# Optimization experiments

Measured on AMD Instinct MI355X. Metric: run time of the kernel, lower is better.

Reference implementation:

```python
import jax, jax.numpy as jnp
import numpy as np

NUM_HEADS = 16
EMB_SIZE = 1024
HEAD_SIZE = 64


def setup_inputs() -> dict:
    key = jax.random.key(0)
    ks = jax.random.split(key, 9)
    H, E, D = NUM_HEADS, EMB_SIZE, HEAD_SIZE
    s = 1.0 / np.sqrt(E)
    X = jax.random.normal(ks[0], (4, 2048, E), dtype=jnp.float32)
    Wq = jax.random.uniform(ks[1], (H, E, D), jnp.float32, -s, s)
    Wk = jax.random.uniform(ks[2], (H, E, D), jnp.float32, -s, s)
    Wv = jax.random.uniform(ks[3], (H, E, D), jnp.float32, -s, s)
    bq = jax.random.uniform(ks[4], (H, D), jnp.float32, -s, s)
    bk = jax.random.uniform(ks[5], (H, D), jnp.float32, -s, s)
    bv = jax.random.uniform(ks[6], (H, D), jnp.float32, -s, s)
    so = 1.0 / np.sqrt(H * D)
    Wo = jax.random.uniform(ks[7], (H * D, E), jnp.float32, -so, so)
    bo = jax.random.uniform(ks[8], (E,), jnp.float32, -so, so)
    return {"X": X, "Wq": Wq, "Wk": Wk, "Wv": Wv, "bq": bq, "bk": bk, "bv": bv, "Wo": Wo, "bo": bo}


def reference(X, Wq, Wk, Wv, bq, bk, bv, Wo, bo):
    B, S, E = X.shape
    H, _, D = Wq.shape
    # per-head projections (batched over heads)
    q = jnp.einsum('bse,hed->bhsd', X, Wq) + bq[None, :, None, :]
    k = jnp.einsum('bse,hed->bhsd', X, Wk) + bk[None, :, None, :]
    v = jnp.einsum('bse,hed->bhsd', X, Wv) + bv[None, :, None, :]
    # causal scaled-dot-product attention
    scores = jnp.einsum('bhsd,bhtd->bhst', q, k) / jnp.sqrt(jnp.float32(D))
    causal = jnp.tril(jnp.ones((S, S), dtype=bool))
    scores = jnp.where(causal[None, None], scores, jnp.float32(-jnp.inf))
    probs = jax.nn.softmax(scores, axis=-1)
    out = jnp.einsum('bhst,bhtd->bhsd', probs, v)
    # concat heads (head h occupies slots [h*D:(h+1)*D]) then output proj
    concat = out.transpose(0, 2, 1, 3).reshape(B, S, H * D)
    # dropout is identity in eval mode
    return concat @ Wo + bo
```

## Files before the change

kernel.cpp:

```cpp
#include <hip/hip_runtime.h>
#include <stdint.h>


typedef float   f32x4  __attribute__((ext_vector_type(4)));
typedef __bf16  bf16x8 __attribute__((ext_vector_type(8)));
typedef short   short8 __attribute__((ext_vector_type(8)));
typedef unsigned short ushort4v __attribute__((ext_vector_type(4)));

typedef __attribute__((address_space(1))) void GV;
typedef __attribute__((address_space(3))) void LV;

#define DEVI static __device__ __forceinline__

DEVI unsigned short f2bf(float f){
  unsigned u = __float_as_uint(f);
  unsigned r = u + 0x7fffu + ((u>>16)&1u);
  return (unsigned short)(r>>16);
}

DEVI unsigned cvt_pk_bf16(float lo, float hi){
  unsigned r;
  asm("v_cvt_pk_bf16_f32 %0, %1, %2" : "=v"(r) : "v"(lo), "v"(hi));
  return r;
}

DEVI void permlane32_swap(unsigned &a, unsigned &b){
  asm volatile("v_permlane32_swap_b32 %0, %1" : "+v"(a), "+v"(b));
}
DEVI void permlane16_swap(unsigned &a, unsigned &b){
  asm volatile("v_permlane16_swap_b32 %0, %1" : "+v"(a), "+v"(b));
}

DEVI void gl_lds16(const void* g, void* l){
  __builtin_amdgcn_global_load_lds((GV*)g, (LV*)l, 16, 0, 0);
}

#define BAR() asm volatile("s_barrier" ::: "memory")

__global__ __launch_bounds__(256) void pack_x(const float* __restrict__ X,
                                              short* __restrict__ Xb){
  int i = blockIdx.x*256 + threadIdx.x;
  const float4* p = (const float4*)(X + (size_t)i*8);
  float4 a = p[0], b = p[1];
  short8 o;
  o[0]=(short)f2bf(a.x); o[1]=(short)f2bf(a.y); o[2]=(short)f2bf(a.z); o[3]=(short)f2bf(a.w);
  o[4]=(short)f2bf(b.x); o[5]=(short)f2bf(b.y); o[6]=(short)f2bf(b.z); o[7]=(short)f2bf(b.w);
  *(short8*)(Xb + (size_t)i*8) = o;
}

__global__ __launch_bounds__(256) void pack_wqkv(const float* __restrict__ Wq,
                                                 const float* __restrict__ Wk,
                                                 const float* __restrict__ Wv,
                                                 short* __restrict__ Wp){
  int t = blockIdx.x*256 + threadIdx.x;
  int n = t >> 7, kc = t & 127;
  int which = n >> 10, hd = n & 1023, h = hd >> 6, d = hd & 63;
  const float* W = which==0 ? Wq : (which==1 ? Wk : Wv);
  const float* src = W + ((size_t)h*1024 + kc*8)*64 + d;
  short8 o;
  #pragma unroll
  for (int j=0;j<8;++j) o[j] = (short)f2bf(src[(size_t)j*64]);
  *(short8*)(Wp + (size_t)n*1024 + kc*8) = o;
}

__global__ __launch_bounds__(256) void pack_wo(const float* __restrict__ Wo,
                                               short* __restrict__ WoT){
  int t = blockIdx.x*256 + threadIdx.x;
  int n = t >> 7, kc = t & 127;
  const float* src = Wo + (size_t)(kc*8)*1024 + n;
  short8 o;
  #pragma unroll
  for (int j=0;j<8;++j) o[j] = (short)f2bf(src[(size_t)j*1024]);
  *(short8*)(WoT + (size_t)n*1024 + kc*8) = o;
}

__global__ __launch_bounds__(512)
void gemm_qkv(const short* __restrict__ A, const short* __restrict__ Bt,
              const float* __restrict__ b0, const float* __restrict__ b1,
              const float* __restrict__ b2,
              short* __restrict__ Qb, short* __restrict__ Kb, short* __restrict__ Vtb)
{
  __shared__ __align__(16) char sm[4][32768];
  const int K2 = 2048;
  int t = threadIdx.x, lane = t & 63, wid = t >> 6;
  int wr = wid >> 2, wc = wid & 3;
  int l15 = lane & 15, l4 = lane >> 4;
  int swz = (blockIdx.x & 7) * 48 + (blockIdx.x >> 3);
  int bm = swz & 31, bn = swz >> 5;
  size_t abase = (size_t)bm * 256 * K2;
  size_t bbase = (size_t)bn * 256 * K2;

  f32x4 acc[8][4] = {};
  bf16x8 af[8], bfr[4];
  const char* sA; const char* sB;

  auto stageA = [&](int kt, char* buf){
    int kb = kt * 64;
    #pragma unroll
    for (int c = 0; c < 2; ++c){
      int x = c*8192 + t*16;
      int r = x >> 6;
      gl_lds16((const char*)A + abase + (size_t)r*K2 + kb + (x & 63), buf + c*8192 + wid*1024);
    }
  };
  auto stageB = [&](int kt, char* buf){
    int kb = kt * 64;
    #pragma unroll
    for (int c = 0; c < 2; ++c){
      int x = c*8192 + t*16;
      int r = x >> 6;
      gl_lds16((const char*)Bt + bbase + (size_t)r*K2 + kb + (x & 63), buf + 16384 + c*8192 + wid*1024);
    }
  };
  auto rd_af = [&](){
    #pragma unroll
    for (int i = 0; i < 8; ++i){
      int ra = wr*128 + i*16 + l15;
      af[i] = *(const bf16x8*)(sA + ra*64 + l4*16);
    }
  };
  auto rd_bf = [&](int j0){
    #pragma unroll
    for (int j = 0; j < 2; ++j){
      int rb = wc*64 + (j0 + j)*16 + l15;
      bfr[j0 + j] = *(const bf16x8*)(sB + rb*64 + l4*16);
    }
  };
  auto mm = [&](int j0){
    __builtin_amdgcn_s_setprio(1);
    #pragma unroll
    for (int i = 0; i < 8; ++i)
      #pragma unroll
      for (int j = 0; j < 2; ++j)
        acc[i][j0+j] = __builtin_amdgcn_mfma_f32_16x16x32_bf16(af[i], bfr[j0+j], acc[i][j0+j], 0, 0, 0);
    __builtin_amdgcn_s_setprio(0);
  };

  stageA(0, sm[0]); stageB(0, sm[0]);
  stageA(1, sm[1]); stageB(1, sm[1]);
  stageA(2, sm[2]); stageB(2, sm[2]);

  for (int kt = 0; kt < 32; ++kt){
    if      (kt < 30) asm volatile("s_waitcnt vmcnt(8)" ::: "memory");
    else if (kt == 30) asm volatile("s_waitcnt vmcnt(4)" ::: "memory");
    else               asm volatile("s_waitcnt vmcnt(0)" ::: "memory");
    BAR();
    sA = sm[kt & 3]; sB = sA + 16384;
    char* nb = sm[(kt + 3) & 3];
    bool st = kt < 29;
    rd_af(); rd_bf(0);
    if (st) stageA(kt + 3, nb);
    BAR(); mm(0); BAR();
    rd_bf(2);
    if (st) stageB(kt + 3, nb);
    BAR(); mm(2);
  }

  #pragma unroll
  for (int i = 0; i < 8; ++i){
    int mbase = bm*256 + wr*128 + i*16 + l4*4;
    #pragma unroll
    for (int j = 0; j < 4; ++j){
      int n = bn*256 + wc*64 + j*16 + l15;
      int which = n >> 10, hd = n & 1023, h = hd >> 6, d = hd & 63;
      const float* bp = which==0 ? b0 : (which==1 ? b1 : b2);
      float bias = bp[hd];
      int b = mbase >> 11, sbase = mbase & 2047;
      size_t bh = (size_t)(b*16 + h);
      if (which == 2){
        ushort4v pv;
        #pragma unroll
        for (int r = 0; r < 4; ++r) pv[r] = f2bf(acc[i][j][r] + bias);
        *(ushort4v*)(Vtb + (bh*64 + d)*2048 + sbase) = pv;
      } else {
        short* dst = (which==0 ? Qb : Kb) + bh*2048*64;
        float sc = which==0 ? 0.18033688f : 1.0f;
        #pragma unroll
        for (int r = 0; r < 4; ++r)
          dst[(size_t)(sbase + r)*64 + d] = (short)f2bf((acc[i][j][r] + bias) * sc);
      }
    }
  }
}

__global__ __launch_bounds__(512)
void gemm_out(const short* __restrict__ A, const short* __restrict__ Bt,
              const float* __restrict__ b0, float* __restrict__ Out)
{
  __shared__ __align__(16) char sm[3][49152];
  const int K2 = 2048;
  int t = threadIdx.x, lane = t & 63, wid = t >> 6;
  int wr = wid >> 2, wc = wid & 3;
  int l15 = lane & 15, l4 = lane >> 4;
  int swz = (blockIdx.x & 7) * 32 + (blockIdx.x >> 3);
  int bm = swz & 63, bn = swz >> 6;
  size_t abase = (size_t)bm * 128 * K2;
  size_t bbase = (size_t)bn * 256 * K2;

  f32x4 acc[4][4] = {};
  const char* sA; const char* sB;
  bf16x8 af[4], bfr[4];

  auto stageA = [&](int kt, char* buf){
    int kb = kt * 128;
    #pragma unroll
    for (int c = 0; c < 2; ++c){
      int x = c*8192 + t*16;
      int r = x >> 7, z = x & 127;
      int zs = z ^ ((r & 7) << 4);
      gl_lds16((const char*)A + abase + (size_t)r*K2 + kb + zs, buf + c*8192 + wid*1024);
    }
  };
  auto stageB = [&](int kt, char* buf, int c0){
    int kb = kt * 128;
    #pragma unroll
    for (int c = 0; c < 2; ++c){
      int cc = c0 + c;
      int x = cc*8192 + t*16;
      int r = x >> 7, z = x & 127;
      int zs = z ^ ((r & 7) << 4);
      gl_lds16((const char*)Bt + bbase + (size_t)r*K2 + kb + zs, buf + 16384 + cc*8192 + wid*1024);
    }
  };
  auto rd_af = [&](int kk){
    int cb = kk*64 + l4*16;
    #pragma unroll
    for (int i = 0; i < 4; ++i){
      int ra = wr*64 + i*16 + l15;
      af[i] = *(const bf16x8*)(sA + ra*128 + (cb ^ ((ra&7)<<4)));
    }
  };
  auto rd_bf = [&](int kk, int j0){
    int cb = kk*64 + l4*16;
    #pragma unroll
    for (int j = 0; j < 2; ++j){
      int rb = wc*64 + (j0 + j)*16 + l15;
      bfr[j0 + j] = *(const bf16x8*)(sB + rb*128 + (cb ^ ((rb&7)<<4)));
    }
  };
  auto mm = [&](int j0){
    __builtin_amdgcn_s_setprio(1);
    #pragma unroll
    for (int i = 0; i < 4; ++i)
      #pragma unroll
      for (int j = 0; j < 2; ++j)
        acc[i][j0+j] = __builtin_amdgcn_mfma_f32_16x16x32_bf16(af[i], bfr[j0+j], acc[i][j0+j], 0, 0, 0);
    __builtin_amdgcn_s_setprio(0);
  };

  stageA(0, sm[0]); stageB(0, sm[0], 0); stageB(0, sm[0], 2);
  stageA(1, sm[1]); stageB(1, sm[1], 0); stageB(1, sm[1], 2);

  for (int kt = 0; kt < 16; ++kt){
    if (kt == 15) asm volatile("s_waitcnt vmcnt(0)" ::: "memory");
    else          asm volatile("s_waitcnt vmcnt(6)" ::: "memory");
    BAR();
    sA = sm[kt % 3]; sB = sA + 16384;
    char* nb = sm[(kt + 2) % 3];
    bool st = kt < 14;
    rd_af(0); rd_bf(0, 0);
    if (st) stageA(kt + 2, nb);
    BAR(); mm(0); BAR();
    rd_bf(0, 2);
    if (st) stageB(kt + 2, nb, 0);
    BAR(); mm(2); BAR();
    rd_af(1); rd_bf(1, 0);
    if (st) stageB(kt + 2, nb, 2);
    BAR(); mm(0); BAR();
    rd_bf(1, 2);
    BAR(); mm(2);
  }

  #pragma unroll
  for (int i = 0; i < 4; ++i){
    int mbase = bm*128 + wr*64 + i*16 + l4*4;
    #pragma unroll
    for (int j = 0; j < 4; ++j){
      int n = bn*256 + wc*64 + j*16 + l15;
      float bias = b0[n];
      #pragma unroll
      for (int r = 0; r < 4; ++r)
        Out[(size_t)(mbase + r)*1024 + n] = acc[i][j][r] + bias;
    }
  }
}

__global__ __launch_bounds__(256, 4)
void attn(const short* __restrict__ Qb, const short* __restrict__ Kb,
          const short* __restrict__ Vtb, short* __restrict__ Ob)
{
  __shared__ __align__(16) char smK[2][8192];
  __shared__ __align__(16) char smV[2][8192];
  int t = threadIdx.x, lane = t & 63, wid = t >> 6;
  int l15 = lane & 15, hi = lane >> 4;
  int hi16 = hi*16, hi4 = hi*4;
  int bh = blockIdx.x & 63;
  int j = blockIdx.x >> 6;
  int qb = (j < 8) ? (15 - j) : (j - 8);
  int b = bh >> 4, h = bh & 15;
  int wq0 = qb*128 + wid*32;
  const char* Qh = (const char*)(Qb + (size_t)bh*2048*64);
  const char* Kh = (const char*)(Kb + (size_t)bh*2048*64);
  const char* Vh = (const char*)(Vtb + (size_t)bh*64*2048);

  bf16x8 vones;
  #pragma unroll
  for (int z = 0; z < 8; ++z) vones[z] = (__bf16)1.0f;

  bf16x8 qf[2][2];
  #pragma unroll
  for (int qt = 0; qt < 2; ++qt)
    #pragma unroll
    for (int kk = 0; kk < 2; ++kk)
      qf[qt][kk] = *(const bf16x8*)(Qh + (size_t)(wq0 + qt*16 + l15)*128 + kk*64 + hi16);

  f32x4 oacc[2][4] = {};
  f32x4 lacc[2] = {};
  float m[2] = {-1e30f, -1e30f};

  int nkt = 2*qb + 2;

  #pragma unroll
  for (int c = 0; c < 2; ++c){
    int x = c*4096 + t*16;
    int r = x >> 7, z = x & 127;
    int zs = z ^ ((r & 7) << 4);
    gl_lds16(Kh + (size_t)r*128 + zs, smK[0] + c*4096 + wid*1024);
    gl_lds16(Vh + (size_t)r*4096 + zs, smV[0] + c*4096 + wid*1024);
  }
  __syncthreads();

  for (int kt = 0; kt < nkt; ++kt){
    int cur = kt & 1;
    if (kt + 1 < nkt){
      int nxt = cur ^ 1;
      #pragma unroll
      for (int c = 0; c < 2; ++c){
        int x = c*4096 + t*16;
        int r = x >> 7, z = x & 127;
        int zs = z ^ ((r & 7) << 4);
        gl_lds16(Kh + (size_t)(kt+1)*8192 + (size_t)r*128 + zs, smK[nxt] + c*4096 + wid*1024);
        gl_lds16(Vh + (size_t)r*4096 + (size_t)(kt+1)*128 + zs, smV[nxt] + c*4096 + wid*1024);
      }
    }
    const char* Kc = smK[cur];
    const char* Vc = smV[cur];
    int kbase = kt * 64;

    #pragma unroll
    for (int qt = 0; qt < 2; ++qt){
      int qlo = wq0 + qt*16;
      if (kbase > qlo + 15) continue;

      f32x4 sa[4];
      __builtin_amdgcn_s_setprio(1);
      #pragma unroll
      for (int nt = 0; nt < 4; ++nt){
        f32x4 a = {};
        #pragma unroll
        for (int kk = 0; kk < 2; ++kk){
          int rk = nt*16 + l15;
          bf16x8 kf = *(const bf16x8*)(Kc + rk*128 + ((kk*64 + hi16) ^ ((rk&7)<<4)));
          a = __builtin_amdgcn_mfma_f32_16x16x32_bf16(kf, qf[qt][kk], a, 0, 0, 0);
        }
        sa[nt] = a;
      }
      __builtin_amdgcn_s_setprio(0);

      if (kbase + 63 > qlo){
        int qrow = qlo + l15;
        #pragma unroll
        for (int nt = 0; nt < 4; ++nt)
          #pragma unroll
          for (int r = 0; r < 4; ++r)
            if (kbase + nt*16 + hi4 + r > qrow) sa[nt][r] = -1e30f;
      }

      float pm;
      {
        float t0 = fmaxf(fmaxf(sa[0][0], sa[0][1]), sa[0][2]);
        float t1 = fmaxf(fmaxf(sa[0][3], sa[1][0]), sa[1][1]);
        float t2 = fmaxf(fmaxf(sa[1][2], sa[1][3]), sa[2][0]);
        float t3 = fmaxf(fmaxf(sa[2][1], sa[2][2]), sa[2][3]);
        float t4 = fmaxf(fmaxf(sa[3][0], sa[3][1]), sa[3][2]);
        float u0 = fmaxf(fmaxf(t0, t1), sa[3][3]);
        float u1 = fmaxf(fmaxf(t2, t3), t4);
        pm = fmaxf(u0, u1);
      }
      pm = fmaxf(pm, __shfl_xor(pm, 16));
      pm = fmaxf(pm, __shfl_xor(pm, 32));
      float mq = m[qt];
      if (!__all(pm <= mq + 8.0f)){
        float mnew = fmaxf(mq, pm);
        float sc = exp2f(mq - mnew);
        lacc[qt] *= sc;
        #pragma unroll
        for (int dt = 0; dt < 4; ++dt) oacc[qt][dt] *= sc;
        m[qt] = mnew; mq = mnew;
      }
      unsigned pw[8];
      #pragma unroll
      for (int nt = 0; nt < 4; ++nt){
        float p0 = exp2f(sa[nt][0] - mq);
        float p1 = exp2f(sa[nt][1] - mq);
        float p2 = exp2f(sa[nt][2] - mq);
        float p3 = exp2f(sa[nt][3] - mq);
        pw[nt*2]   = cvt_pk_bf16(p0, p1);
        pw[nt*2+1] = cvt_pk_bf16(p2, p3);
      }

      union U { unsigned u[4]; bf16x8 v; } f0, f1;
      {
        unsigned a0 = pw[0], b0v = pw[2];
        permlane32_swap(a0, b0v); permlane16_swap(a0, b0v);
        unsigned a1 = pw[1], b1v = pw[3];
        permlane32_swap(a1, b1v); permlane16_swap(a1, b1v);
        f0.u[0] = a0; f0.u[1] = a1; f0.u[2] = b0v; f0.u[3] = b1v;
        unsigned a2 = pw[4], b2v = pw[6];
        permlane32_swap(a2, b2v); permlane16_swap(a2, b2v);
        unsigned a3 = pw[5], b3v = pw[7];
        permlane32_swap(a3, b3v); permlane16_swap(a3, b3v);
        f1.u[0] = a2; f1.u[1] = a3; f1.u[2] = b2v; f1.u[3] = b3v;
      }

      __builtin_amdgcn_s_setprio(1);
      #pragma unroll
      for (int kk = 0; kk < 2; ++kk){
        bf16x8 pf = kk ? f1.v : f0.v;
        lacc[qt] = __builtin_amdgcn_mfma_f32_16x16x32_bf16(vones, pf, lacc[qt], 0, 0, 0);
        #pragma unroll
        for (int dt = 0; dt < 4; ++dt){
          int rv = dt*16 + l15;
          bf16x8 vf = *(const bf16x8*)(Vc + rv*128 + ((kk*64 + hi16) ^ ((rv&7)<<4)));
          oacc[qt][dt] = __builtin_amdgcn_mfma_f32_16x16x32_bf16(vf, pf, oacc[qt][dt], 0, 0, 0);
        }
      }
      __builtin_amdgcn_s_setprio(0);
    }
    __syncthreads();
  }

  #pragma unroll
  for (int qt = 0; qt < 2; ++qt){
    float inv = 1.0f / lacc[qt][0];
    int srow = wq0 + qt*16 + l15;
    size_t rb = ((size_t)(b*2048 + srow))*1024 + h*64 + hi4;
    #pragma unroll
    for (int dt = 0; dt < 4; ++dt){
      unsigned w0 = cvt_pk_bf16(oacc[qt][dt][0]*inv, oacc[qt][dt][1]*inv);
      unsigned w1 = cvt_pk_bf16(oacc[qt][dt][2]*inv, oacc[qt][dt][3]*inv);
      *(unsigned long long*)(Ob + rb + dt*16) =
          ((unsigned long long)w1 << 32) | (unsigned long long)w0;
    }
  }
}

extern "C" void kernel_launch(void* const* d_in, const int* in_sizes, int n_in,
                              void* d_out, int out_size, void* d_ws, size_t ws_size,
                              hipStream_t stream)
{
  const float* X  = (const float*)d_in[0];
  const float* Wq = (const float*)d_in[1];
  const float* Wk = (const float*)d_in[2];
  const float* Wv = (const float*)d_in[3];
  const float* bq = (const float*)d_in[4];
  const float* bk = (const float*)d_in[5];
  const float* bv = (const float*)d_in[6];
  const float* Wo = (const float*)d_in[7];
  const float* bo = (const float*)d_in[8];
  float* Out = (float*)d_out;

  char* ws = (char*)d_ws;
  short* Xbf  = (short*)(ws);
  short* Wp   = (short*)(ws + 16777216);
  short* WoT  = (short*)(ws + 23068672);
  short* Qb   = (short*)(ws + 25165824);
  short* Kb   = (short*)(ws + 41943040);
  short* Vtb  = (short*)(ws + 58720256);
  short* Ob   = (short*)(ws + 75497472);

  pack_x   <<<4096, 256, 0, stream>>>(X, Xbf);
  pack_wqkv<<<1536, 256, 0, stream>>>(Wq, Wk, Wv, Wp);
  pack_wo  <<< 512, 256, 0, stream>>>(Wo, WoT);

  gemm_qkv<<<384, 512, 0, stream>>>(Xbf, Wp, bq, bk, bv, Qb, Kb, Vtb);
  attn    <<<1024, 256, 0, stream>>>(Qb, Kb, Vtb, Ob);
  gemm_out<<<256, 512, 0, stream>>>(Ob, WoT, bo, Out);
}
```

Baseline: 212.6 us.

## Double-buffer QKV GEMM with 128-wide K tiles and XOR-swizzled LDS

Restructures the QKV projection GEMM mainloop from a 4-stage, 64-wide K pipeline into a 2-stage double buffer with 128-wide K tiles, issuing the full next tile's loads before computing the current one. It applies an XOR swizzle on LDS rows to avoid bank conflicts on the wider 128-byte rows. It also removes the mid-iteration barriers and split MFMA halves. This reduces barrier count and the number of loop iterations but shrinks prefetch depth, which may expose global-load latency.

```diff
diff --git a/kernel.cpp b/kernel.cpp
--- a/kernel.cpp
+++ b/kernel.cpp
@@ -80,7 +80,7 @@
               const float* __restrict__ b2,
               short* __restrict__ Qb, short* __restrict__ Kb, short* __restrict__ Vtb)
 {
-  __shared__ __align__(16) char sm[4][32768];
+  __shared__ __align__(16) char sm[2][65536];
   const int K2 = 2048;
   int t = threadIdx.x, lane = t & 63, wid = t >> 6;
   int wr = wid >> 2, wc = wid & 3;
@@ -95,65 +95,68 @@
   const char* sA; const char* sB;
 
   auto stageA = [&](int kt, char* buf){
-    int kb = kt * 64;
-    #pragma unroll
-    for (int c = 0; c < 2; ++c){
+    int kb = kt * 128;
+    #pragma unroll
+    for (int c = 0; c < 4; ++c){
       int x = c*8192 + t*16;
-      int r = x >> 6;
-      gl_lds16((const char*)A + abase + (size_t)r*K2 + kb + (x & 63), buf + c*8192 + wid*1024);
+      int r = x >> 7, z = x & 127;
+      int zs = z ^ ((r & 7) << 4);
+      gl_lds16((const char*)A + abase + (size_t)r*K2 + kb + zs, buf + c*8192 + wid*1024);
     }
   };
   auto stageB = [&](int kt, char* buf){
-    int kb = kt * 64;
-    #pragma unroll
-    for (int c = 0; c < 2; ++c){
+    int kb = kt * 128;
+    #pragma unroll
+    for (int c = 0; c < 4; ++c){
       int x = c*8192 + t*16;
-      int r = x >> 6;
-      gl_lds16((const char*)Bt + bbase + (size_t)r*K2 + kb + (x & 63), buf + 16384 + c*8192 + wid*1024);
-    }
-  };
-  auto rd_af = [&](){
+      int r = x >> 7, z = x & 127;
+      int zs = z ^ ((r & 7) << 4);
+      gl_lds16((const char*)Bt + bbase + (size_t)r*K2 + kb + zs, buf + 32768 + c*8192 + wid*1024);
+    }
+  };
+  auto rd_af = [&](int kk){
+    int cb = kk*64 + l4*16;
     #pragma unroll
     for (int i = 0; i < 8; ++i){
       int ra = wr*128 + i*16 + l15;
-      af[i] = *(const bf16x8*)(sA + ra*64 + l4*16);
-    }
-  };
-  auto rd_bf = [&](int j0){
-    #pragma unroll
-    for (int j = 0; j < 2; ++j){
-      int rb = wc*64 + (j0 + j)*16 + l15;
-      bfr[j0 + j] = *(const bf16x8*)(sB + rb*64 + l4*16);
-    }
-  };
-  auto mm = [&](int j0){
+      af[i] = *(const bf16x8*)(sA + ra*128 + (cb ^ ((ra&7)<<4)));
+    }
+  };
+  auto rd_bf = [&](int kk){
+    int cb = kk*64 + l4*16;
+    #pragma unroll
+    for (int j = 0; j < 4; ++j){
+      int rb = wc*64 + j*16 + l15;
+      bfr[j] = *(const bf16x8*)(sB + rb*128 + (cb ^ ((rb&7)<<4)));
+    }
+  };
+  auto mm = [&](){
     __builtin_amdgcn_s_setprio(1);
     #pragma unroll
     for (int i = 0; i < 8; ++i)
       #pragma unroll
-      for (int j = 0; j < 2; ++j)
-        acc[i][j0+j] = __builtin_amdgcn_mfma_f32_16x16x32_bf16(af[i], bfr[j0+j], acc[i][j0+j], 0, 0, 0);
+      for (int j = 0; j < 4; ++j)
+        acc[i][j] = __builtin_amdgcn_mfma_f32_16x16x32_bf16(af[i], bfr[j], acc[i][j], 0, 0, 0);
     __builtin_amdgcn_s_setprio(0);
   };
 
   stageA(0, sm[0]); stageB(0, sm[0]);
-  stageA(1, sm[1]); stageB(1, sm[1]);
-  stageA(2, sm[2]); stageB(2, sm[2]);
-
-  for (int kt = 0; kt < 32; ++kt){
-    if      (kt < 30) asm volatile("s_waitcnt vmcnt(8)" ::: "memory");
-    else if (kt == 30) asm volatile("s_waitcnt vmcnt(4)" ::: "memory");
-    else               asm volatile("s_waitcnt vmcnt(0)" ::: "memory");
+
+  for (int kt = 0; kt < 16; ++kt){
     BAR();
-    sA = sm[kt & 3]; sB = sA + 16384;
-    char* nb = sm[(kt + 3) & 3];
-    bool st = kt < 29;
-    rd_af(); rd_bf(0);
-    if (st) stageA(kt + 3, nb);
-    BAR(); mm(0); BAR();
-    rd_bf(2);
-    if (st) stageB(kt + 3, nb);
-    BAR(); mm(2);
+    if (kt < 15){
+      char* nb = sm[(kt + 1) & 1];
+      stageA(kt + 1, nb); stageB(kt + 1, nb);
+      asm volatile("s_waitcnt vmcnt(8)" ::: "memory");
+    } else {
+      asm volatile("s_waitcnt vmcnt(0)" ::: "memory");
+    }
+    BAR();
+    sA = sm[kt & 1]; sB = sA + 32768;
+    rd_af(0); rd_bf(0);
+    mm();
+    rd_af(1); rd_bf(1);
+    mm();
   }
 
   #pragma unroll
```

Measured after the change: 203.5 us. 4.3% less time.
